# Kernel tuning notes

Hardware: AMD Instinct MI355X
Metric: run time of the kernel (lower is better)

The kernel has to match this reference:

```python
import jax, jax.numpy as jnp
import numpy as np

H = 8          # num_heads_temporal_attn
ROPE_BASE = 10000.0


def _rope_cos_sin(seq_len, head_dim, dtype):
    # RotaryEmbedding1D: per-head rotary over head_dim
    inv_freq = 1.0 / (ROPE_BASE ** (jnp.arange(0, head_dim, 2, dtype=jnp.float32) / head_dim))
    freqs = jnp.arange(seq_len, dtype=jnp.float32)[:, None] * inv_freq[None, :]  # (S, hd/2)
    emb = jnp.concatenate([freqs, freqs], axis=-1)  # (S, hd)
    return jnp.cos(emb).astype(dtype), jnp.sin(emb).astype(dtype)


def _rotate_half(x):
    half = x.shape[-1] // 2
    return jnp.concatenate([-x[..., half:], x[..., :half]], axis=-1)


def _forward(hidden_states, qkv_w, qkv_b, proj_w, proj_b, cu_seqlens):
    B, T, N, D = hidden_states.shape
    S = B * T * N
    hd = D // H
    scaling = hd ** (-0.5)

    x = hidden_states.reshape(S, D)
    qkv = x @ qkv_w + qkv_b                      # (S, 3D)
    qkv = qkv.reshape(S, 3, H, hd)
    q, k, v = qkv[:, 0], qkv[:, 1], qkv[:, 2]    # each (S, H, hd)

    cos, sin = _rope_cos_sin(S, hd, x.dtype)     # (S, hd)
    cos, sin = cos[:, None, :], sin[:, None, :]  # broadcast over heads
    q = q * cos + _rotate_half(q) * sin
    k = k * cos + _rotate_half(k) * sin

    # scores: (H, S, S)
    scores = jnp.einsum('shd,thd->hst', q, k) * scaling

    # block-diagonal mask from cu_seqlens (bucketize == searchsorted side='left')
    seq_id = jnp.searchsorted(cu_seqlens[1:-1], jnp.arange(S, dtype=cu_seqlens.dtype), side='left')
    same = seq_id[:, None] == seq_id[None, :]    # (S, S)
    scores = jnp.where(same[None, :, :], scores, -jnp.inf)

    attn = jax.nn.softmax(scores.astype(jnp.float32), axis=-1).astype(q.dtype)  # (H, S, S)
    out = jnp.einsum('hst,thd->shd', attn, v).reshape(S, H * hd)
    out = out @ proj_w + proj_b
    final = out.reshape(B, T, N, D)
    return final, attn[None]  # attn_weights with leading batch dim (1, H, S, S)


def setup_inputs() -> dict:
    key = jax.random.key(0)
    ks = jax.random.split(key, 5)
    B, T, N, D = 1, 16, 256, 512
    hidden_states = jax.random.normal(ks[0], (B, T, N, D), dtype=jnp.float32)
    qkv_w = jax.random.normal(ks[1], (D, 3 * D), dtype=jnp.float32) * 0.02
    qkv_b = jnp.zeros((3 * D,), dtype=jnp.float32)
    proj_w = jax.random.normal(ks[2], (D, D), dtype=jnp.float32) * 0.02
    proj_b = jnp.zeros((D,), dtype=jnp.float32)
    cu_seqlens = jnp.array([0, 1024, 2560, 4096], dtype=jnp.int32)  # 3 packed videos
    return {"hidden_states": hidden_states, "qkv_w": qkv_w, "qkv_b": qkv_b,
            "proj_w": proj_w, "proj_b": proj_b, "cu_seqlens": cu_seqlens}


def reference(hidden_states, qkv_w, qkv_b, proj_w, proj_b, cu_seqlens):
    return _forward(hidden_states, qkv_w, qkv_b, proj_w, proj_b, cu_seqlens)
```

## Files before the change

### kernel.cpp

```cpp
#include <hip/hip_runtime.h>
#include <math.h>

typedef short bf16x8 __attribute__((ext_vector_type(8)));
typedef float f32x4 __attribute__((ext_vector_type(4)));
typedef unsigned short u16x8 __attribute__((ext_vector_type(8)));


__device__ __forceinline__ unsigned short f2b(float f) {
  union { float f; unsigned int u; } v; v.f = f;
  unsigned int u = v.u;
  return (unsigned short)((u + 0x7FFFu + ((u >> 16) & 1u)) >> 16);
}
__device__ __forceinline__ float b2f(unsigned short h) {
  union { unsigned int u; float f; } v; v.u = ((unsigned int)h) << 16; return v.f;
}

__global__ __launch_bounds__(256) void k_tables(float* __restrict__ cosT, float* __restrict__ sinT) {
  int idx = blockIdx.x * 256 + threadIdx.x;
  if (idx >= 4096 * 32) return;
  int pos = idx >> 5, i = idx & 31;
  float invf = (float)(1.0 / pow(10000.0, (double)i / 32.0));
  float ang = (float)pos * invf;
  cosT[idx] = cosf(ang);
  sinT[idx] = sinf(ang);
}

__global__ __launch_bounds__(256) void k_vpad(unsigned short* __restrict__ vT) {
  int h = blockIdx.x, t = threadIdx.x;
  for (int i = t; i < 64 * 64; i += 256) {
    int d = i >> 6, c = i & 63;
    vT[((size_t)(h * 64 + d)) * 4160 + 1024 + c] = 0;
  }
  if (t < 64) vT[((size_t)(h * 64 + t)) * 4160 + 4159] = 0;
}

__global__ __launch_bounds__(256) void k_cvt(const float* __restrict__ x, unsigned short* __restrict__ xb, int n4) {
  int idx = blockIdx.x * 256 + threadIdx.x;
  if (idx >= n4) return;
  float4 v = ((const float4*)x)[idx];
  ushort4 o; o.x = f2b(v.x); o.y = f2b(v.y); o.z = f2b(v.z); o.w = f2b(v.w);
  ((ushort4*)xb)[idx] = o;
}

__global__ __launch_bounds__(256) void k_twcvt(const float* __restrict__ src, unsigned short* __restrict__ dst,
                                               int K, int N) {
  __shared__ float tile[32][33];
  int k0 = blockIdx.x * 32, n0 = blockIdx.y * 32;
  int t = threadIdx.x;
  for (int i = 0; i < 4; i++) {
    int e = t + i * 256; int r = e >> 5, c = e & 31;
    tile[r][c] = src[(size_t)(k0 + r) * N + n0 + c];
  }
  __syncthreads();
  for (int i = 0; i < 4; i++) {
    int e = t + i * 256; int r = e >> 5, c = e & 31;
    dst[(size_t)(n0 + r) * K + k0 + c] = f2b(tile[c][r]);
  }
}

__global__ __launch_bounds__(256) void k_gemm(const unsigned short* __restrict__ A,
                                              const unsigned short* __restrict__ Bt,
                                              const float* __restrict__ bias,
                                              float* __restrict__ C,
                                              int M, int N, int K) {
  __shared__ unsigned short As[64][72];
  __shared__ unsigned short Bs[64][72];
  int row0 = blockIdx.x * 64, col0 = blockIdx.y * 64;
  int t = threadIdx.x, w = t >> 6, l = t & 63;
  int l15 = l & 15, l4 = l >> 4;
  f32x4 acc[4] = {};
  for (int k0 = 0; k0 < K; k0 += 64) {
    for (int i = 0; i < 2; i++) {
      int e = t + i * 256; int r = e >> 3, c8 = e & 7;
      *(uint4*)&As[r][c8 * 8] = *(const uint4*)(A + (size_t)(row0 + r) * K + k0 + c8 * 8);
      *(uint4*)&Bs[r][c8 * 8] = *(const uint4*)(Bt + (size_t)(col0 + r) * K + k0 + c8 * 8);
    }
    __syncthreads();
    for (int kh = 0; kh < 2; kh++) {
      bf16x8 a = *(const bf16x8*)&As[w * 16 + l15][kh * 32 + l4 * 8];
      for (int cf = 0; cf < 4; cf++) {
        bf16x8 b = *(const bf16x8*)&Bs[cf * 16 + l15][kh * 32 + l4 * 8];
        acc[cf] = __builtin_amdgcn_mfma_f32_16x16x32_bf16(a, b, acc[cf], 0, 0, 0);
      }
    }
    __syncthreads();
  }
  for (int cf = 0; cf < 4; cf++) {
    int col = col0 + cf * 16 + l15;
    float bv = bias[col];
    for (int r = 0; r < 4; r++) {
      int row = row0 + w * 16 + l4 * 4 + r;
      C[(size_t)row * N + col] = acc[cf][r] + bv;
    }
  }
}

__global__ __launch_bounds__(256) void k_gemm_qkv(const unsigned short* __restrict__ A,
                                                  const unsigned short* __restrict__ Bt,
                                                  const float* __restrict__ bias,
                                                  const float* __restrict__ cosT,
                                                  const float* __restrict__ sinT,
                                                  unsigned short* __restrict__ qh,
                                                  unsigned short* __restrict__ kh,
                                                  unsigned short* __restrict__ vT) {
  __shared__ unsigned short As[64][72];
  __shared__ unsigned short Bs[64][72];
  int row0 = blockIdx.x * 64, col0 = blockIdx.y * 64;
  int t = threadIdx.x, w = t >> 6, l = t & 63;
  int l15 = l & 15, l4 = l >> 4;
  f32x4 acc[4] = {};
  for (int k0 = 0; k0 < 512; k0 += 64) {
    for (int i = 0; i < 2; i++) {
      int e = t + i * 256; int r = e >> 3, c8 = e & 7;
      *(uint4*)&As[r][c8 * 8] = *(const uint4*)(A + (size_t)(row0 + r) * 512 + k0 + c8 * 8);
      *(uint4*)&Bs[r][c8 * 8] = *(const uint4*)(Bt + (size_t)(col0 + r) * 512 + k0 + c8 * 8);
    }
    __syncthreads();
    for (int kk = 0; kk < 2; kk++) {
      bf16x8 a = *(const bf16x8*)&As[w * 16 + l15][kk * 32 + l4 * 8];
      for (int cf = 0; cf < 4; cf++) {
        bf16x8 b = *(const bf16x8*)&Bs[cf * 16 + l15][kk * 32 + l4 * 8];
        acc[cf] = __builtin_amdgcn_mfma_f32_16x16x32_bf16(a, b, acc[cf], 0, 0, 0);
      }
    }
    __syncthreads();
  }
  for (int cf = 0; cf < 4; cf++) {
    float bv = bias[col0 + cf * 16 + l15];
    for (int r = 0; r < 4; r++) acc[cf][r] += bv;
  }
  int kind = col0 >> 9;
  int h = (col0 & 511) >> 6;
  if (kind < 2) {
    for (int r = 0; r < 4; r++) {
      int row = row0 + w * 16 + l4 * 4 + r;
      float c0 = cosT[row * 32 + l15],      s0 = sinT[row * 32 + l15];
      float c1 = cosT[row * 32 + 16 + l15], s1 = sinT[row * 32 + 16 + l15];
      float q0 = acc[0][r], q1 = acc[1][r], q2 = acc[2][r], q3 = acc[3][r];
      int rl = w * 16 + l4 * 4 + r;
      As[rl][0 * 16 + l15] = f2b(q0 * c0 - q2 * s0);
      As[rl][1 * 16 + l15] = f2b(q1 * c1 - q3 * s1);
      As[rl][2 * 16 + l15] = f2b(q2 * c0 + q0 * s0);
      As[rl][3 * 16 + l15] = f2b(q3 * c1 + q1 * s1);
    }
  } else {
    for (int cf = 0; cf < 4; cf++)
      for (int r = 0; r < 4; r++)
        As[w * 16 + l4 * 4 + r][cf * 16 + l15] = f2b(acc[cf][r]);
  }
  __syncthreads();
  if (kind < 2) {
    unsigned short* dst = (kind == 0 ? qh : kh);
    for (int p = 0; p < 2; p++) {
      int idx = p * 256 + t;
      int rl = idx >> 3, c8 = (idx & 7) * 8;
      *(u16x8*)(dst + ((size_t)(h * 4096 + row0 + rl)) * 64 + c8) = *(const u16x8*)&As[rl][c8];
    }
  } else {
    for (int p = 0; p < 2; p++) {
      int idx = p * 256 + t;
      int d = idx >> 3, s8 = (idx & 7) * 8;
      int sbase = row0 + s8;
      u16x8 val;
      for (int j = 0; j < 8; j++) val[j] = As[s8 + j][d];
      unsigned short* vrow = vT + ((size_t)(h * 64 + d)) * 4160;
      if (sbase != 1024) {
        int pc = (sbase < 1025) ? sbase : sbase + 63;
        *(u16x8*)(vrow + pc) = val;
      } else {
        for (int j = 0; j < 8; j++) {
          int s = sbase + j;
          vrow[(s < 1025) ? s : s + 63] = val[j];
        }
      }
    }
  }
}

template<int SEG>
__device__ __forceinline__ void attn_body(int h, int row0,
    const unsigned short* __restrict__ qh, const unsigned short* __restrict__ kh,
    const unsigned short* __restrict__ vT, float* __restrict__ attn,
    unsigned short* __restrict__ opre,
    unsigned short (&Ks)[64][72], unsigned short (&Vt)[64][72],
    unsigned short (&Sc)[32][72], float (&pd)[4][16], float (&dn)[32],
    float (&carry)[2][32]) {
  constexpr int LO  = SEG == 0 ? 0 : (SEG == 1 ? 1025 : 2561);
  constexpr int HI  = SEG == 0 ? 1025 : (SEG == 1 ? 2561 : 4096);
  constexpr int LEN = HI - LO;
  constexpr int NKT = SEG == 0 ? 17 : 24;
  constexpr int CS  = SEG == 0 ? 0 : (SEG == 1 ? 1088 : 2624);
  constexpr int CQ0 = LO & ~3;
  constexpr int DLO = LO - CQ0;
  constexpr int ZQ  = SEG == 0 ? 752 : (SEG == 1 ? 639 : 640);
  constexpr int QPT = SEG == 0 ? 3 : 2;

  int t = threadIdx.x, w = t >> 6, l = t & 63, l15 = l & 15, l4 = l >> 4;
  int rw = (w & 1) * 16, ch = (w >> 1) * 32;

  int nvalid = HI - row0; if (nvalid > 32) nvalid = 32;
  int Z = nvalid * ZQ;
  int zc = t;
  float* abase = attn + ((size_t)h * 4096 + row0) * 4096;
  float4 z4 = make_float4(0.f, 0.f, 0.f, 0.f);

  auto zero_step = [&]() {
    for (int j = 0; j < QPT; j++) {
      int z = zc; zc += 256;
      if (z < Z) {
        int row = z / ZQ, qi = z - row * ZQ;
        int q = SEG == 0 ? qi + 272 : (SEG == 1 ? (qi < 256 ? qi : qi + 385) : qi);
        *(float4*)(abase + (size_t)row * 4096 + q * 4) = z4;
      }
    }
  };

  bf16x8 qa[2];
  {
    int m = row0 + rw + l15; if (m > 4095) m = 4095;
    const unsigned short* qp = qh + ((size_t)(h * 4096 + m)) * 64;
    qa[0] = *(const bf16x8*)(qp + l4 * 8);
    qa[1] = *(const bf16x8*)(qp + 32 + l4 * 8);
  }

  float rsum[4] = {0.f, 0.f, 0.f, 0.f};
  for (int ct = 0; ct < NKT; ct++) {
    for (int i = 0; i < 2; i++) {
      int e = t + i * 256; int r = e >> 3, c8 = e & 7;
      int kr = LO + ct * 64 + r; if (kr > 4095) kr = 4095;
      *(uint4*)&Ks[r][c8 * 8] = *(const uint4*)(kh + ((size_t)(h * 4096 + kr)) * 64 + c8 * 8);
    }
    zero_step();
    __syncthreads();
    f32x4 acc[2] = {};
    for (int kf = 0; kf < 2; kf++)
      for (int cf = 0; cf < 2; cf++) {
        bf16x8 b = *(const bf16x8*)&Ks[ch + cf * 16 + l15][kf * 32 + l4 * 8];
        acc[cf] = __builtin_amdgcn_mfma_f32_16x16x32_bf16(qa[kf], b, acc[cf], 0, 0, 0);
      }
    for (int cf = 0; cf < 2; cf++) {
      int gc = ct * 64 + ch + cf * 16 + l15;
      bool valid = gc < LEN;
      for (int r = 0; r < 4; r++)
        rsum[r] += valid ? __expf(acc[cf][r] * 0.125f) : 0.f;
    }
    __syncthreads();
  }
  for (int r = 0; r < 4; r++) {
    float s = rsum[r];
    for (int o = 1; o < 16; o <<= 1) s += __shfl_xor(s, o, 16);
    rsum[r] = s;
  }
  if (l15 == 0)
    for (int r = 0; r < 4; r++) pd[w][l4 * 4 + r] = rsum[r];
  __syncthreads();
  if (t < 32) {
    int half = t >> 4, rr = t & 15;
    dn[t] = 1.f / (pd[half][rr] + pd[half + 2][rr]);
  }
  __syncthreads();

  f32x4 pacc[2] = {};
  for (int ct = 0; ct < NKT; ct++) {
    for (int i = 0; i < 2; i++) {
      int e = t + i * 256; int r = e >> 3, c8 = e & 7;
      int kr = LO + ct * 64 + r; if (kr > 4095) kr = 4095;
      *(uint4*)&Ks[r][c8 * 8] = *(const uint4*)(kh + ((size_t)(h * 4096 + kr)) * 64 + c8 * 8);
      *(uint4*)&Vt[r][c8 * 8] = *(const uint4*)(vT + ((size_t)(h * 64 + r)) * 4160 + CS + ct * 64 + c8 * 8);
    }
    zero_step();
    __syncthreads();
    f32x4 acc[2] = {};
    for (int kf = 0; kf < 2; kf++)
      for (int cf = 0; cf < 2; cf++) {
        bf16x8 b = *(const bf16x8*)&Ks[ch + cf * 16 + l15][kf * 32 + l4 * 8];
        acc[cf] = __builtin_amdgcn_mfma_f32_16x16x32_bf16(qa[kf], b, acc[cf], 0, 0, 0);
      }
    for (int cf = 0; cf < 2; cf++)
      for (int r = 0; r < 4; r++)
        Sc[rw + l4 * 4 + r][ch + cf * 16 + l15] = f2b(__expf(acc[cf][r] * 0.125f));
    __syncthreads();
    for (int j = 0; j < 2; j++) {
      int idx = w * 128 + j * 64 + l;
      int row = idx >> 4, qt = idx & 15;
      int grow = row0 + row;
      if (grow < HI) {
        float inv = dn[row];
        float4 o; float* po = &o.x;
        for (int k = 0; k < 4; k++) {
          int c = qt * 4 - DLO + k;
          float v = 0.f;
          if (c >= 0) {
            if (ct * 64 + c < LEN) v = b2f(Sc[row][c]) * inv;
          } else if (ct > 0) {
            v = carry[(ct & 1) ^ 1][row];
          }
          po[k] = v;
        }
        *(float4*)(abase + (size_t)row * 4096 + CQ0 + ct * 64 + qt * 4) = o;
      }
    }
    if (DLO == 1 && t < 32) {
      int grow = row0 + t;
      if (grow < HI) carry[ct & 1][t] = b2f(Sc[t][63]) * dn[t];
    }
    for (int kf = 0; kf < 2; kf++) {
      bf16x8 ap = *(const bf16x8*)&Sc[rw + l15][kf * 32 + l4 * 8];
      for (int cf = 0; cf < 2; cf++) {
        bf16x8 b = *(const bf16x8*)&Vt[ch + cf * 16 + l15][kf * 32 + l4 * 8];
        pacc[cf] = __builtin_amdgcn_mfma_f32_16x16x32_bf16(ap, b, pacc[cf], 0, 0, 0);
      }
    }
    __syncthreads();
  }
  if (SEG == 1 && t < 32) {
    int grow = row0 + t;
    if (grow < HI)
      *(float4*)(abase + (size_t)t * 4096 + 2560) = make_float4(carry[(NKT - 1) & 1][t], 0.f, 0.f, 0.f);
  }

  for (int cf = 0; cf < 2; cf++)
    for (int r = 0; r < 4; r++) {
      int lrow = rw + l4 * 4 + r;
      int grow = row0 + lrow;
      if (grow < HI)
        opre[(size_t)grow * 512 + h * 64 + ch + cf * 16 + l15] = f2b(pacc[cf][r] * dn[lrow]);
    }
}

__global__ __launch_bounds__(256) void k_attn3(const unsigned short* __restrict__ qh,
                                               const unsigned short* __restrict__ kh,
                                               const unsigned short* __restrict__ vT,
                                               float* __restrict__ attn,
                                               unsigned short* __restrict__ opre) {
  __shared__ unsigned short Ks[64][72];
  __shared__ unsigned short Vt[64][72];
  __shared__ unsigned short Sc[32][72];
  __shared__ float pd[4][16];
  __shared__ float dn[32];
  __shared__ float carry[2][32];
  int bid = blockIdx.x;
  int h = bid / 129, st = bid % 129;
  if (st < 33)      attn_body<0>(h, st * 32,               qh, kh, vT, attn, opre, Ks, Vt, Sc, pd, dn, carry);
  else if (st < 81) attn_body<1>(h, 1025 + (st - 33) * 32, qh, kh, vT, attn, opre, Ks, Vt, Sc, pd, dn, carry);
  else              attn_body<2>(h, 2561 + (st - 81) * 32, qh, kh, vT, attn, opre, Ks, Vt, Sc, pd, dn, carry);
}

extern "C" void kernel_launch(void* const* d_in, const int* in_sizes, int n_in,
                              void* d_out, int out_size, void* d_ws, size_t ws_size,
                              hipStream_t stream) {
  const float* hidden = (const float*)d_in[0];
  const float* qkv_w  = (const float*)d_in[1];
  const float* qkv_b  = (const float*)d_in[2];
  const float* proj_w = (const float*)d_in[3];
  const float* proj_b = (const float*)d_in[4];

  char* p = (char*)d_ws;
  auto alloc = [&](size_t bytes) { char* r = p; p += (bytes + 255) & ~(size_t)255; return r; };
  float*          cosT   = (float*)alloc((size_t)4096 * 32 * 4);
  float*          sinT   = (float*)alloc((size_t)4096 * 32 * 4);
  unsigned short* xb     = (unsigned short*)alloc((size_t)4096 * 512 * 2);
  unsigned short* wqkvT  = (unsigned short*)alloc((size_t)1536 * 512 * 2);
  unsigned short* wprojT = (unsigned short*)alloc((size_t)512 * 512 * 2);
  unsigned short* qhb    = (unsigned short*)alloc((size_t)8 * 4096 * 64 * 2);
  unsigned short* khb    = (unsigned short*)alloc((size_t)8 * 4096 * 64 * 2);
  unsigned short* vTb    = (unsigned short*)alloc((size_t)8 * 64 * 4160 * 2);
  unsigned short* opre   = (unsigned short*)alloc((size_t)4096 * 512 * 2);

  float* final_out = (float*)d_out;
  float* attn_out  = (float*)d_out + (size_t)4096 * 512;

  k_tables<<<dim3(512), dim3(256), 0, stream>>>(cosT, sinT);
  k_vpad<<<dim3(8), dim3(256), 0, stream>>>(vTb);
  k_cvt<<<dim3(2048), dim3(256), 0, stream>>>(hidden, xb, 4096 * 512 / 4);
  k_twcvt<<<dim3(16, 48), dim3(256), 0, stream>>>(qkv_w, wqkvT, 512, 1536);
  k_twcvt<<<dim3(16, 16), dim3(256), 0, stream>>>(proj_w, wprojT, 512, 512);
  k_gemm_qkv<<<dim3(64, 24), dim3(256), 0, stream>>>(xb, wqkvT, qkv_b, cosT, sinT, qhb, khb, vTb);
  k_attn3<<<dim3(8 * 129), dim3(256), 0, stream>>>(qhb, khb, vTb, attn_out, opre);
  k_gemm<<<dim3(64, 8), dim3(256), 0, stream>>>(opre, wprojT, proj_b, final_out, 4096, 512, 512);
}
```

Baseline: 182.3 us.

## Split softmax denominator pass into separate kernel before attention output kernel

```diff
diff --git a/kernel.cpp b/kernel.cpp
--- a/kernel.cpp
+++ b/kernel.cpp
@@ -178,13 +178,84 @@
 }
 
 template<int SEG>
-__device__ __forceinline__ void attn_body(int h, int row0,
+__device__ __forceinline__ void dn_body(int h, int row0,
     const unsigned short* __restrict__ qh, const unsigned short* __restrict__ kh,
-    const unsigned short* __restrict__ vT, float* __restrict__ attn,
-    unsigned short* __restrict__ opre,
+    float* __restrict__ Dn,
+    unsigned short (&Ks)[64][72], float (&pd)[4][16]) {
+  constexpr int LO  = SEG == 0 ? 0 : (SEG == 1 ? 1025 : 2561);
+  constexpr int HI  = SEG == 0 ? 1025 : (SEG == 1 ? 2561 : 4096);
+  constexpr int LEN = HI - LO;
+  constexpr int NKT = SEG == 0 ? 17 : 24;
+
+  int t = threadIdx.x, w = t >> 6, l = t & 63, l15 = l & 15, l4 = l >> 4;
+  int rw = (w & 1) * 16, ch = (w >> 1) * 32;
+
+  bf16x8 qa[2];
+  {
+    int m = row0 + rw + l15; if (m > 4095) m = 4095;
+    const unsigned short* qp = qh + ((size_t)(h * 4096 + m)) * 64;
+    qa[0] = *(const bf16x8*)(qp + l4 * 8);
+    qa[1] = *(const bf16x8*)(qp + 32 + l4 * 8);
+  }
+
+  float rsum[4] = {0.f, 0.f, 0.f, 0.f};
+  for (int ct = 0; ct < NKT; ct++) {
+    for (int i = 0; i < 2; i++) {
+      int e = t + i * 256; int r = e >> 3, c8 = e & 7;
+      int kr = LO + ct * 64 + r; if (kr > 4095) kr = 4095;
+      *(uint4*)&Ks[r][c8 * 8] = *(const uint4*)(kh + ((size_t)(h * 4096 + kr)) * 64 + c8 * 8);
+    }
+    __syncthreads();
+    f32x4 acc[2] = {};
+    for (int kf = 0; kf < 2; kf++)
+      for (int cf = 0; cf < 2; cf++) {
+        bf16x8 b = *(const bf16x8*)&Ks[ch + cf * 16 + l15][kf * 32 + l4 * 8];
+        acc[cf] = __builtin_amdgcn_mfma_f32_16x16x32_bf16(qa[kf], b, acc[cf], 0, 0, 0);
+      }
+    for (int cf = 0; cf < 2; cf++) {
+      int gc = ct * 64 + ch + cf * 16 + l15;
+      bool valid = gc < LEN;
+      for (int r = 0; r < 4; r++)
+        rsum[r] += valid ? __expf(acc[cf][r] * 0.125f) : 0.f;
+    }
+    __syncthreads();
+  }
+  for (int r = 0; r < 4; r++) {
+    float s = rsum[r];
+    for (int o = 1; o < 16; o <<= 1) s += __shfl_xor(s, o, 16);
+    rsum[r] = s;
+  }
+  if (l15 == 0)
+    for (int r = 0; r < 4; r++) pd[w][l4 * 4 + r] = rsum[r];
+  __syncthreads();
+  if (t < 32) {
+    int grow = row0 + t;
+    if (grow < HI) {
+      int half = t >> 4, rr = t & 15;
+      Dn[h * 4096 + grow] = 1.f / (pd[half][rr] + pd[half + 2][rr]);
+    }
+  }
+}
+
+__global__ __launch_bounds__(256) void k_dn(const unsigned short* __restrict__ qh,
+                                            const unsigned short* __restrict__ kh,
+                                            float* __restrict__ Dn) {
+  __shared__ unsigned short Ks[64][72];
+  __shared__ float pd[4][16];
+  int bid = blockIdx.x;
+  int h = bid / 129, st = bid % 129;
+  if (st < 33)      dn_body<0>(h, st * 32,               qh, kh, Dn, Ks, pd);
+  else if (st < 81) dn_body<1>(h, 1025 + (st - 33) * 32, qh, kh, Dn, Ks, pd);
+  else              dn_body<2>(h, 2561 + (st - 81) * 32, qh, kh, Dn, Ks, pd);
+}
+
+template<int SEG>
+__device__ __forceinline__ void attn_body4(int h, int row0,
+    const unsigned short* __restrict__ qh, const unsigned short* __restrict__ kh,
+    const unsigned short* __restrict__ vT, const float* __restrict__ Dn,
+    float* __restrict__ attn, unsigned short* __restrict__ opre,
     unsigned short (&Ks)[64][72], unsigned short (&Vt)[64][72],
-    unsigned short (&Sc)[32][72], float (&pd)[4][16], float (&dn)[32],
-    float (&carry)[2][32]) {
+    unsigned short (&Sc)[32][72], float (&dn)[32], float (&carry)[2][32]) {
   constexpr int LO  = SEG == 0 ? 0 : (SEG == 1 ? 1025 : 2561);
   constexpr int HI  = SEG == 0 ? 1025 : (SEG == 1 ? 2561 : 4096);
   constexpr int LEN = HI - LO;
@@ -193,7 +264,7 @@
   constexpr int CQ0 = LO & ~3;
   constexpr int DLO = LO - CQ0;
   constexpr int ZQ  = SEG == 0 ? 752 : (SEG == 1 ? 639 : 640);
-  constexpr int QPT = SEG == 0 ? 3 : 2;
+  constexpr int QPT = SEG == 0 ? 6 : 4;
 
   int t = threadIdx.x, w = t >> 6, l = t & 63, l15 = l & 15, l4 = l >> 4;
   int rw = (w & 1) * 16, ch = (w >> 1) * 32;
@@ -215,6 +286,11 @@
     }
   };
 
+  if (t < 32) {
+    int grow = row0 + t;
+    dn[t] = (grow < HI) ? Dn[h * 4096 + grow] : 0.f;
+  }
+
   bf16x8 qa[2];
   {
     int m = row0 + rw + l15; if (m > 4095) m = 4095;
@@ -222,43 +298,6 @@
     qa[0] = *(const bf16x8*)(qp + l4 * 8);
     qa[1] = *(const bf16x8*)(qp + 32 + l4 * 8);
   }
-
-  float rsum[4] = {0.f, 0.f, 0.f, 0.f};
-  for (int ct = 0; ct < NKT; ct++) {
-    for (int i = 0; i < 2; i++) {
-      int e = t + i * 256; int r = e >> 3, c8 = e & 7;
-      int kr = LO + ct * 64 + r; if (kr > 4095) kr = 4095;
-      *(uint4*)&Ks[r][c8 * 8] = *(const uint4*)(kh + ((size_t)(h * 4096 + kr)) * 64 + c8 * 8);
-    }
-    zero_step();
-    __syncthreads();
-    f32x4 acc[2] = {};
-    for (int kf = 0; kf < 2; kf++)
-      for (int cf = 0; cf < 2; cf++) {
-        bf16x8 b = *(const bf16x8*)&Ks[ch + cf * 16 + l15][kf * 32 + l4 * 8];
-        acc[cf] = __builtin_amdgcn_mfma_f32_16x16x32_bf16(qa[kf], b, acc[cf], 0, 0, 0);
-      }
-    for (int cf = 0; cf < 2; cf++) {
-      int gc = ct * 64 + ch + cf * 16 + l15;
-      bool valid = gc < LEN;
-      for (int r = 0; r < 4; r++)
-        rsum[r] += valid ? __expf(acc[cf][r] * 0.125f) : 0.f;
-    }
-    __syncthreads();
-  }
-  for (int r = 0; r < 4; r++) {
-    float s = rsum[r];
-    for (int o = 1; o < 16; o <<= 1) s += __shfl_xor(s, o, 16);
-    rsum[r] = s;
-  }
-  if (l15 == 0)
-    for (int r = 0; r < 4; r++) pd[w][l4 * 4 + r] = rsum[r];
-  __syncthreads();
-  if (t < 32) {
-    int half = t >> 4, rr = t & 15;
-    dn[t] = 1.f / (pd[half][rr] + pd[half + 2][rr]);
-  }
-  __syncthreads();
 
   f32x4 pacc[2] = {};
   for (int ct = 0; ct < NKT; ct++) {
@@ -328,22 +367,22 @@
     }
 }
 
-__global__ __launch_bounds__(256) void k_attn3(const unsigned short* __restrict__ qh,
+__global__ __launch_bounds__(256) void k_attn4(const unsigned short* __restrict__ qh,
                                                const unsigned short* __restrict__ kh,
                                                const unsigned short* __restrict__ vT,
+                                               const float* __restrict__ Dn,
                                                float* __restrict__ attn,
                                                unsigned short* __restrict__ opre) {
   __shared__ unsigned short Ks[64][72];
   __shared__ unsigned short Vt[64][72];
   __shared__ unsigned short Sc[32][72];
-  __shared__ float pd[4][16];
   __shared__ float dn[32];
   __shared__ float carry[2][32];
   int bid = blockIdx.x;
   int h = bid / 129, st = bid % 129;
-  if (st < 33)      attn_body<0>(h, st * 32,               qh, kh, vT, attn, opre, Ks, Vt, Sc, pd, dn, carry);
-  else if (st < 81) attn_body<1>(h, 1025 + (st - 33) * 32, qh, kh, vT, attn, opre, Ks, Vt, Sc, pd, dn, carry);
-  else              attn_body<2>(h, 2561 + (st - 81) * 32, qh, kh, vT, attn, opre, Ks, Vt, Sc, pd, dn, carry);
+  if (st < 33)      attn_body4<0>(h, st * 32,               qh, kh, vT, Dn, attn, opre, Ks, Vt, Sc, dn, carry);
+  else if (st < 81) attn_body4<1>(h, 1025 + (st - 33) * 32, qh, kh, vT, Dn, attn, opre, Ks, Vt, Sc, dn, carry);
+  else              attn_body4<2>(h, 2561 + (st - 81) * 32, qh, kh, vT, Dn, attn, opre, Ks, Vt, Sc, dn, carry);
 }
 
 extern "C" void kernel_launch(void* const* d_in, const int* in_sizes, int n_in,
@@ -366,6 +405,7 @@
   unsigned short* khb    = (unsigned short*)alloc((size_t)8 * 4096 * 64 * 2);
   unsigned short* vTb    = (unsigned short*)alloc((size_t)8 * 64 * 4160 * 2);
   unsigned short* opre   = (unsigned short*)alloc((size_t)4096 * 512 * 2);
+  float*          Dnb    = (float*)alloc((size_t)8 * 4096 * 4);
 
   float* final_out = (float*)d_out;
   float* attn_out  = (float*)d_out + (size_t)4096 * 512;
@@ -376,6 +416,7 @@
   k_twcvt<<<dim3(16, 48), dim3(256), 0, stream>>>(qkv_w, wqkvT, 512, 1536);
   k_twcvt<<<dim3(16, 16), dim3(256), 0, stream>>>(proj_w, wprojT, 512, 512);
   k_gemm_qkv<<<dim3(64, 24), dim3(256), 0, stream>>>(xb, wqkvT, qkv_b, cosT, sinT, qhb, khb, vTb);
-  k_attn3<<<dim3(8 * 129), dim3(256), 0, stream>>>(qhb, khb, vTb, attn_out, opre);
+  k_dn<<<dim3(8 * 129), dim3(256), 0, stream>>>(qhb, khb, Dnb);
+  k_attn4<<<dim3(8 * 129), dim3(256), 0, stream>>>(qhb, khb, vTb, Dnb, attn_out, opre);
   k_gemm<<<dim3(64, 8), dim3(256), 0, stream>>>(opre, wprojT, proj_b, final_out, 4096, 512, 512);
 }
```

New measurement: 199.1 us. +9.3%, slower.
